# Performance work log

Hardware: AMD Instinct MI355X
Metric: run time of the kernel (lower is better)

## Reference

```python
import jax, jax.numpy as jnp
import numpy as np

B, CIN, COUT, K, S, P, D = 4, 128, 128, 3, 1, 1, 1
H = W = 96
MASK_SCALE = 2.0


def setup_inputs() -> dict:
    key = jax.random.key(0)
    k1, k2, k3, k4 = jax.random.split(key, 4)
    x = jax.random.normal(k1, (B, CIN, H, W), jnp.float32)
    weight = jax.random.normal(k2, (COUT, CIN, K, K), jnp.float32) * 0.05
    bias = jax.random.normal(k3, (COUT,), jnp.float32) * 0.05
    # conv_offset_mask: out_channels = deformable_groups*3*K*K = 27, no bias
    w_offmask = jax.random.normal(k4, (3 * K * K, CIN, K, K), jnp.float32) * 0.01
    return {"x": x, "weight": weight, "bias": bias, "w_offmask": w_offmask}


def _bilinear_gather(x, py, px):
    """x: [B,C,H,W]; py,px: [B,K2,Ho,Wo] float sample coords.
    Returns [B,C,K2,Ho,Wo], zero outside image (per-corner validity as in DCNv2)."""
    Bn, C, Hh, Ww = x.shape
    K2, Ho, Wo = py.shape[1], py.shape[2], py.shape[3]
    y0 = jnp.floor(py); x0 = jnp.floor(px)
    ly = py - y0; lx = px - x0
    y0i = y0.astype(jnp.int32); x0i = x0.astype(jnp.int32)
    y1i = y0i + 1; x1i = x0i + 1
    x_flat = x.reshape(Bn, C, Hh * Ww)

    def corner(yi, xi, w):
        valid = (yi >= 0) & (yi < Hh) & (xi >= 0) & (xi < Ww)
        yc = jnp.clip(yi, 0, Hh - 1)
        xc = jnp.clip(xi, 0, Ww - 1)
        idx = (yc * Ww + xc).reshape(Bn, K2 * Ho * Wo)
        v = jnp.take_along_axis(x_flat, idx[:, None, :], axis=2)  # [B,C,K2*Ho*Wo]
        v = v.reshape(Bn, C, K2, Ho, Wo)
        wv = (w * valid.astype(x.dtype))[:, None]  # [B,1,K2,Ho,Wo]
        return v * wv

    out = corner(y0i, x0i, (1 - ly) * (1 - lx))
    out = out + corner(y0i, x1i, (1 - ly) * lx)
    out = out + corner(y1i, x0i, ly * (1 - lx))
    out = out + corner(y1i, x1i, ly * lx)
    return out


def reference(x, weight, bias, w_offmask):
    K2 = K * K
    # offset/mask conv (standard conv, no bias)
    om = jax.lax.conv_general_dilated(
        x, w_offmask, window_strides=(S, S), padding=[(P, P), (P, P)],
        dimension_numbers=("NCHW", "OIHW", "NCHW"))  # [B, 3*K2, Ho, Wo]
    o1 = om[:, :K2]
    o2 = om[:, K2:2 * K2]
    mask = jax.nn.sigmoid(om[:, 2 * K2:]) * MASK_SCALE  # [B,K2,Ho,Wo]
    offset = jnp.concatenate([o1, o2], axis=1)  # [B,2*K2,Ho,Wo]

    Ho, Wo = om.shape[2], om.shape[3]
    ki, kj = jnp.meshgrid(jnp.arange(K), jnp.arange(K), indexing="ij")
    ki = ki.reshape(K2); kj = kj.reshape(K2)
    ho = jnp.arange(Ho); wo = jnp.arange(Wo)
    base_y = (ho[None, :] * S - P + ki[:, None] * D).astype(x.dtype)  # [K2,Ho]
    base_x = (wo[None, :] * S - P + kj[:, None] * D).astype(x.dtype)  # [K2,Wo]
    py = base_y[None, :, :, None] + o1  # [B,K2,Ho,Wo]
    px = base_x[None, :, None, :] + o2

    sampled = _bilinear_gather(x, py, px)            # [B,C,K2,Ho,Wo]
    sampled = sampled * mask[:, None]                # modulation
    wr = weight.reshape(COUT, CIN, K2)
    out = jnp.einsum("ock,bckhw->bohw", wr, sampled) + bias[None, :, None, None]
    return out, offset
```

## Files before the change

### kernel.cpp

```cpp
#include <hip/hip_runtime.h>
#include <math.h>

#define HH 96
#define WW 96
#define HW (96*96)
#define CIN_ 128
#define COUT_ 128
#define OUT_ELEMS (4*128*96*96)
#define TPX 48

#define XT_OFF   0u
#define WBF_OFF  9437184u
#define WOMB_OFF 9732096u

typedef __attribute__((ext_vector_type(8))) short short8v;
typedef __attribute__((ext_vector_type(4))) float float4v;

__device__ __forceinline__ unsigned short f2bf(float f) {
    unsigned u = __builtin_bit_cast(unsigned, f);
    u += 0x7FFFu + ((u >> 16) & 1u);
    return (unsigned short)(u >> 16);
}
__device__ __forceinline__ unsigned rneu(float f) {
    unsigned u = __builtin_bit_cast(unsigned, f);
    return u + 0x7FFFu + ((u >> 16) & 1u);
}
__device__ __forceinline__ unsigned pkbf(float hi, float lo) {
    return __builtin_amdgcn_perm(rneu(hi), rneu(lo), 0x07060302u);
}
__device__ __forceinline__ float bflo(unsigned u) {
    return __builtin_bit_cast(float, u << 16);
}
__device__ __forceinline__ float bfhi(unsigned u) {
    return __builtin_bit_cast(float, u & 0xffff0000u);
}

__global__ __launch_bounds__(256) void pre_kernel(
    const float* __restrict__ x, const float* __restrict__ w,
    const float* __restrict__ wom, unsigned short* __restrict__ xt,
    unsigned short* __restrict__ wbf, unsigned short* __restrict__ womb)
{
    __shared__ float tile[64][130];
    const int t = threadIdx.x;
    const int f = blockIdx.x;

    if (f < 576) {
        const int g  = (f & 7) * 72 + (f >> 3);
        const int b  = g / 144;
        const int p0 = (g - b * 144) * 64;
#pragma unroll
        for (int j = 0; j < 8; j++) {
            const int i  = j * 256 + t;
            const int c  = i >> 4;
            const int p4 = (i & 15) * 4;
            const float4 v = *(const float4*)(x + ((size_t)(b * CIN_ + c) * HW + p0 + p4));
            tile[p4 + 0][c] = v.x; tile[p4 + 1][c] = v.y;
            tile[p4 + 2][c] = v.z; tile[p4 + 3][c] = v.w;
        }
        __syncthreads();
#pragma unroll
        for (int j = 0; j < 8; j++) {
            const int i   = j * 256 + t;
            const int pxl = i >> 5;
            const int c4  = (i & 31) * 4;
            uint2 v;
            v.x = pkbf(tile[pxl][c4 + 1], tile[pxl][c4 + 0]);
            v.y = pkbf(tile[pxl][c4 + 3], tile[pxl][c4 + 2]);
            *(uint2*)(xt + ((size_t)(b * HW + p0 + pxl) * CIN_ + c4)) = v;
        }
    } else {
        const int i = (f - 576) * 256 + t;
        if (i < COUT_ * 1152) {
            const int oc = i / 1152, r = i - oc * 1152;
            const int kc = r >> 7, c = r & 127;
            wbf[i] = f2bf(w[(size_t)oc * 1152 + c * 9 + kc]);
        } else {
            const int i2 = i - COUT_ * 1152;
            if (i2 < 32 * 1152) {
                const int row = i2 / 1152, r = i2 - row * 1152;
                const int kc = r >> 7, c = r & 127;
                womb[i2] = (row < 27) ? f2bf(wom[(size_t)row * 1152 + c * 9 + kc]) : 0;
            }
        }
    }
}

__global__ __launch_bounds__(512, 6) void dconv_fused(
    const unsigned short* __restrict__ xt, const unsigned short* __restrict__ wbf,
    const unsigned short* __restrict__ womb, const float* __restrict__ bias,
    float* __restrict__ out, float* __restrict__ off_out)
{
    __shared__ int smem[9600];
    int*   sprep  = smem;
    int*   btile0 = smem + 3456;
    int*   btile1 = smem + 6528;
    float* som    = (float*)btile0;

    const int t    = threadIdx.x;
    const int wave = __builtin_amdgcn_readfirstlane(t >> 6);
    const int lane = t & 63;
    const int quad = lane >> 4;
    const int m    = lane & 15;
    const int l32  = lane & 31;
    const int half = lane >> 5;

    const int f  = blockIdx.x;
    const int c  = (f & 7) * 96 + (f >> 3);
    const int b  = c / 192;
    const int p0 = (c - b * 192) * TPX;

    const unsigned short* xtb = xt + (size_t)b * HW * CIN_;

    if (wave < 6) {
        const int pxg = wave >> 1;
        const int mt  = wave & 1;
        const int pgl = pxg * 16 + m;
        const int pg  = p0 + pgl;
        const int h   = pg / 96;
        const int w   = pg - h * 96;

        float4v acc2;
#pragma unroll
        for (int r = 0; r < 4; r++) acc2[r] = 0.f;
        const short8v zerov = (short8v)0;

#pragma unroll
        for (int kc = 0; kc < 9; kc++) {
            const int ki = kc / 3, kj = kc - 3 * (kc / 3);
            const int y  = h + ki - 1, xx = w + kj - 1;
            const bool valid = ((unsigned)y < 96u) && ((unsigned)xx < 96u);
            const unsigned short* brow = xtb + (size_t)(y * 96 + xx) * CIN_ + quad * 8;
            const short* abase = (const short*)womb + (size_t)(mt * 16 + m) * 1152 + kc * 128 + quad * 8;
#pragma unroll
            for (int kst = 0; kst < 4; kst++) {
                const short8v bfv = valid ? *(const short8v*)(brow + kst * 32) : zerov;
                const short8v av  = *(const short8v*)(abase + kst * 32);
                acc2 = __builtin_amdgcn_mfma_f32_16x16x32_bf16(av, bfv, acc2, 0, 0, 0);
            }
        }
#pragma unroll
        for (int r = 0; r < 4; r++) {
            const int oc = mt * 16 + quad * 4 + r;
            if (oc < 27) som[oc * TPX + pgl] = acc2[r];
            if (oc < 18) off_out[(size_t)(b * 18 + oc) * HW + pg] = acc2[r];
        }
    }
    __syncthreads();

    if (t < 432) {
        const int kc  = t / 48;
        const int pxl = t - kc * 48;
        const int pg  = p0 + pxl;
        const int h   = pg / 96;
        const int w   = pg - h * 96;
        const int ki  = kc / 3, kj = kc - 3 * (kc / 3);

        const float o1 = som[kc * TPX + pxl];
        const float o2 = som[(9 + kc) * TPX + pxl];
        const float mr = som[(18 + kc) * TPX + pxl];
        const float mk = 2.f / (1.f + __expf(-mr));

        const float py = (float)(h - 1 + ki) + o1;
        const float px = (float)(w - 1 + kj) + o2;
        const float y0f = floorf(py), x0f = floorf(px);
        const float ly = py - y0f,    lx = px - x0f;
        const int y0 = (int)y0f, x0 = (int)x0f;
        const int y1 = y0 + 1,   x1 = x0 + 1;

        const float w00 = (1.f - ly) * (1.f - lx), w01 = (1.f - ly) * lx;
        const float w10 = ly * (1.f - lx),         w11 = ly * lx;

        const int yc0 = min(max(y0, 0), HH - 1), yc1 = min(max(y1, 0), HH - 1);
        const int xc0 = min(max(x0, 0), WW - 1), xc1 = min(max(x1, 0), WW - 1);
        const bool vy0 = (y0 >= 0) && (y0 < HH), vy1 = (y1 >= 0) && (y1 < HH);
        const bool vx0 = (x0 >= 0) && (x0 < WW), vx1 = (x1 >= 0) && (x1 < WW);

        sprep[t * 8 + 0] = yc0 * 96 + xc0;
        sprep[t * 8 + 1] = yc0 * 96 + xc1;
        sprep[t * 8 + 2] = yc1 * 96 + xc0;
        sprep[t * 8 + 3] = yc1 * 96 + xc1;
        sprep[t * 8 + 4] = __builtin_bit_cast(int, (vy0 && vx0) ? mk * w00 : 0.f);
        sprep[t * 8 + 5] = __builtin_bit_cast(int, (vy0 && vx1) ? mk * w01 : 0.f);
        sprep[t * 8 + 6] = __builtin_bit_cast(int, (vy1 && vx0) ? mk * w10 : 0.f);
        sprep[t * 8 + 7] = __builtin_bit_cast(int, (vy1 && vx1) ? mk * w11 : 0.f);
    }
    __syncthreads();

    uint2 gbuf[3][4];

#define ISSUE(SL, KCV, ITV) do {                                              \
    const int pxl_ = wave * 6 + (ITV) * 2 + half;                             \
    const int4 id4_ = *(const int4*)&sprep[((KCV) * 48 + pxl_) * 8];          \
    const unsigned co_ = (unsigned)l32 << 3;                                  \
    gbuf[SL][0] = *(const uint2*)((const char*)xtb + (((unsigned)id4_.x << 8) | co_)); \
    gbuf[SL][1] = *(const uint2*)((const char*)xtb + (((unsigned)id4_.y << 8) | co_)); \
    gbuf[SL][2] = *(const uint2*)((const char*)xtb + (((unsigned)id4_.z << 8) | co_)); \
    gbuf[SL][3] = *(const uint2*)((const char*)xtb + (((unsigned)id4_.w << 8) | co_)); \
} while (0)

#define COMBINE(SL, IV) do {                                                  \
    const int pxl_ = wave * 6 + (IV) * 2 + half;                              \
    const float4 w4_ = *(const float4*)&sprep[(kc * 48 + pxl_) * 8 + 4];      \
    const uint2 u0 = gbuf[SL][0], u1 = gbuf[SL][1];                           \
    const uint2 u2 = gbuf[SL][2], u3 = gbuf[SL][3];                           \
    const float v0 = w4_.x*bflo(u0.x) + w4_.y*bflo(u1.x) + w4_.z*bflo(u2.x) + w4_.w*bflo(u3.x); \
    const float v1 = w4_.x*bfhi(u0.x) + w4_.y*bfhi(u1.x) + w4_.z*bfhi(u2.x) + w4_.w*bfhi(u3.x); \
    const float v2 = w4_.x*bflo(u0.y) + w4_.y*bflo(u1.y) + w4_.z*bflo(u2.y) + w4_.w*bflo(u3.y); \
    const float v3 = w4_.x*bfhi(u0.y) + w4_.y*bfhi(u1.y) + w4_.z*bfhi(u2.y) + w4_.w*bfhi(u3.y); \
    uint2 o_;                                                                 \
    o_.x = pkbf(v1, v0);                                                      \
    o_.y = pkbf(v3, v2);                                                      \
    *(uint2*)&bt[pxl_ * 64 + (((l32 >> 1) ^ (pxl_ & 7)) << 2) + ((l32 & 1) << 1)] = o_; \
} while (0)

    float4v acc[3];
#pragma unroll
    for (int j = 0; j < 3; j++)
#pragma unroll
        for (int r = 0; r < 4; r++) acc[j][r] = 0.f;

    ISSUE(0, 0, 0);
    ISSUE(1, 0, 1);
    ISSUE(2, 0, 2);

    for (int kc = 0; kc < 9; kc++) {
        int* bt = (kc & 1) ? btile1 : btile0;

        const short* abase = (const short*)wbf + (size_t)(wave * 16 + m) * 1152 + kc * 128 + quad * 8;
        short8v af[4];
#pragma unroll
        for (int kst = 0; kst < 4; kst++)
            af[kst] = *(const short8v*)(abase + kst * 32);

        COMBINE(0, 0);
        if (kc < 8) ISSUE(0, kc + 1, 0);
        COMBINE(1, 1);
        if (kc < 8) ISSUE(1, kc + 1, 1);
        COMBINE(2, 2);
        if (kc < 8) ISSUE(2, kc + 1, 2);
        __syncthreads();

#pragma unroll
        for (int kst = 0; kst < 4; kst++) {
#pragma unroll
            for (int nt = 0; nt < 3; nt++) {
                const int pxl = nt * 16 + m;
                const short8v bfv = *(const short8v*)((const short*)bt
                    + 2 * (pxl * 64 + (((kst * 4 + quad) ^ (m & 7)) << 2)));
                acc[nt] = __builtin_amdgcn_mfma_f32_16x16x32_bf16(af[kst], bfv, acc[nt], 0, 0, 0);
            }
        }
    }
#undef ISSUE
#undef COMBINE

#pragma unroll
    for (int r = 0; r < 4; r++) {
        const int oc = wave * 16 + quad * 4 + r;
        const float bv = bias[oc];
#pragma unroll
        for (int nt = 0; nt < 3; nt++)
            out[(size_t)(b * COUT_ + oc) * HW + p0 + nt * 16 + m] = acc[nt][r] + bv;
    }
}

extern "C" void kernel_launch(void* const* d_in, const int* in_sizes, int n_in,
                              void* d_out, int out_size, void* d_ws, size_t ws_size,
                              hipStream_t stream) {
    const float* x      = (const float*)d_in[0];
    const float* weight = (const float*)d_in[1];
    const float* bias   = (const float*)d_in[2];
    const float* wom    = (const float*)d_in[3];

    float* out     = (float*)d_out;
    float* off_out = out + OUT_ELEMS;

    unsigned short* xtb  = (unsigned short*)((char*)d_ws + XT_OFF);
    unsigned short* wbf  = (unsigned short*)((char*)d_ws + WBF_OFF);
    unsigned short* womb = (unsigned short*)((char*)d_ws + WOMB_OFF);

    pre_kernel <<<dim3(1296), 256, 0, stream>>>(x, weight, wom, xtb, wbf, womb);
    dconv_fused<<<dim3(768),  512, 0, stream>>>(xtb, wbf, womb, bias, out, off_out);
}
```

Before: 160.2 us.

## Fuse preprocessing and deformable conv into one kernel with grid barrier

Merges the bf16 transpose/weight-conversion kernel into the main deformable conv kernel and separates the two phases with a global atomic grid barrier instead of a second launch. A memset resets the barrier counter before each launch. It also replaces the per-K-chunk __syncthreads with a hand-written LDS wait plus s_barrier that skips waiting on outstanding global loads. This is meant to remove one kernel launch and its tail gap. The risks are that the grid barrier deadlocks unless all 768 blocks are co-resident, and that the memset adds an operation of its own.

```diff
diff --git a/kernel.cpp b/kernel.cpp
--- a/kernel.cpp
+++ b/kernel.cpp
@@ -8,10 +8,12 @@
 #define COUT_ 128
 #define OUT_ELEMS (4*128*96*96)
 #define TPX 48
+#define NBLK 768
 
 #define XT_OFF   0u
 #define WBF_OFF  9437184u
 #define WOMB_OFF 9732096u
+#define BAR_OFF  9805824u
 
 typedef __attribute__((ext_vector_type(8))) short short8v;
 typedef __attribute__((ext_vector_type(4))) float float4v;
@@ -35,22 +37,32 @@
     return __builtin_bit_cast(float, u & 0xffff0000u);
 }
 
-__global__ __launch_bounds__(256) void pre_kernel(
-    const float* __restrict__ x, const float* __restrict__ w,
-    const float* __restrict__ wom, unsigned short* __restrict__ xt,
-    unsigned short* __restrict__ wbf, unsigned short* __restrict__ womb)
+#define BLOCK_SYNC() do {                                   \
+    __builtin_amdgcn_sched_barrier(0);                      \
+    asm volatile("s_waitcnt lgkmcnt(0)" ::: "memory");      \
+    __builtin_amdgcn_s_barrier();                           \
+    __builtin_amdgcn_sched_barrier(0);                      \
+} while (0)
+
+__global__ __launch_bounds__(512, 6) void fused_all(
+    const float* __restrict__ x, const float* __restrict__ weight,
+    const float* __restrict__ bias, const float* __restrict__ wom,
+    float* __restrict__ out, float* __restrict__ off_out,
+    unsigned short* __restrict__ xt, unsigned short* __restrict__ wbf,
+    unsigned short* __restrict__ womb, unsigned int* __restrict__ bar)
 {
-    __shared__ float tile[64][130];
+    __shared__ int smem[9600];
     const int t = threadIdx.x;
     const int f = blockIdx.x;
 
     if (f < 576) {
+        float (*tile)[130] = (float(*)[130])smem;
         const int g  = (f & 7) * 72 + (f >> 3);
         const int b  = g / 144;
         const int p0 = (g - b * 144) * 64;
 #pragma unroll
-        for (int j = 0; j < 8; j++) {
-            const int i  = j * 256 + t;
+        for (int j = 0; j < 4; j++) {
+            const int i  = j * 512 + t;
             const int c  = i >> 4;
             const int p4 = (i & 15) * 4;
             const float4 v = *(const float4*)(x + ((size_t)(b * CIN_ + c) * HW + p0 + p4));
@@ -59,8 +71,8 @@
         }
         __syncthreads();
 #pragma unroll
-        for (int j = 0; j < 8; j++) {
-            const int i   = j * 256 + t;
+        for (int j = 0; j < 4; j++) {
+            const int i   = j * 512 + t;
             const int pxl = i >> 5;
             const int c4  = (i & 31) * 4;
             uint2 v;
@@ -69,34 +81,40 @@
             *(uint2*)(xt + ((size_t)(b * HW + p0 + pxl) * CIN_ + c4)) = v;
         }
     } else {
-        const int i = (f - 576) * 256 + t;
-        if (i < COUT_ * 1152) {
-            const int oc = i / 1152, r = i - oc * 1152;
-            const int kc = r >> 7, c = r & 127;
-            wbf[i] = f2bf(w[(size_t)oc * 1152 + c * 9 + kc]);
-        } else {
-            const int i2 = i - COUT_ * 1152;
-            if (i2 < 32 * 1152) {
-                const int row = i2 / 1152, r = i2 - row * 1152;
+        const int base = (f - 576) * 1024;
+#pragma unroll
+        for (int k = 0; k < 2; k++) {
+            const int i = base + k * 512 + t;
+            if (i < COUT_ * 1152) {
+                const int oc = i / 1152, r = i - oc * 1152;
                 const int kc = r >> 7, c = r & 127;
-                womb[i2] = (row < 27) ? f2bf(wom[(size_t)row * 1152 + c * 9 + kc]) : 0;
+                wbf[i] = f2bf(weight[(size_t)oc * 1152 + c * 9 + kc]);
+            } else {
+                const int i2 = i - COUT_ * 1152;
+                if (i2 < 32 * 1152) {
+                    const int row = i2 / 1152, r = i2 - row * 1152;
+                    const int kc = r >> 7, c = r & 127;
+                    womb[i2] = (row < 27) ? f2bf(wom[(size_t)row * 1152 + c * 9 + kc]) : 0;
+                }
             }
         }
     }
-}
-
-__global__ __launch_bounds__(512, 6) void dconv_fused(
-    const unsigned short* __restrict__ xt, const unsigned short* __restrict__ wbf,
-    const unsigned short* __restrict__ womb, const float* __restrict__ bias,
-    float* __restrict__ out, float* __restrict__ off_out)
-{
-    __shared__ int smem[9600];
+
+    __syncthreads();
+    if (t == 0) {
+        __threadfence();
+        __hip_atomic_fetch_add(bar, 1u, __ATOMIC_ACQ_REL, __HIP_MEMORY_SCOPE_AGENT);
+        while (__hip_atomic_load(bar, __ATOMIC_RELAXED, __HIP_MEMORY_SCOPE_AGENT) < NBLK)
+            __builtin_amdgcn_s_sleep(2);
+        __threadfence();
+    }
+    __syncthreads();
+
     int*   sprep  = smem;
     int*   btile0 = smem + 3456;
     int*   btile1 = smem + 6528;
     float* som    = (float*)btile0;
 
-    const int t    = threadIdx.x;
     const int wave = __builtin_amdgcn_readfirstlane(t >> 6);
     const int lane = t & 63;
     const int quad = lane >> 4;
@@ -104,7 +122,6 @@
     const int l32  = lane & 31;
     const int half = lane >> 5;
 
-    const int f  = blockIdx.x;
     const int c  = (f & 7) * 96 + (f >> 3);
     const int b  = c / 192;
     const int p0 = (c - b * 192) * TPX;
@@ -238,7 +255,8 @@
         if (kc < 8) ISSUE(1, kc + 1, 1);
         COMBINE(2, 2);
         if (kc < 8) ISSUE(2, kc + 1, 2);
-        __syncthreads();
+
+        BLOCK_SYNC();
 
 #pragma unroll
         for (int kst = 0; kst < 4; kst++) {
@@ -278,7 +296,9 @@
     unsigned short* xtb  = (unsigned short*)((char*)d_ws + XT_OFF);
     unsigned short* wbf  = (unsigned short*)((char*)d_ws + WBF_OFF);
     unsigned short* womb = (unsigned short*)((char*)d_ws + WOMB_OFF);
-
-    pre_kernel <<<dim3(1296), 256, 0, stream>>>(x, weight, wom, xtb, wbf, womb);
-    dconv_fused<<<dim3(768),  512, 0, stream>>>(xtb, wbf, womb, bias, out, off_out);
-}
+    unsigned int*   bar  = (unsigned int*)((char*)d_ws + BAR_OFF);
+
+    hipMemsetAsync((void*)bar, 0, 64, stream);
+    fused_all<<<dim3(NBLK), 512, 0, stream>>>(x, weight, bias, wom, out, off_out,
+                                              xtb, wbf, womb, bar);
+}
```

After: 244.1 us. +52.4%, slower.
